# Performance work log

Hardware: AMD Instinct MI355X
Metric: run time of the kernel (lower is better)

Reference implementation:

```python
import jax, jax.numpy as jnp
import numpy as np
from jax import lax

IMG = 800.0      # image size (square)
STRIDE = 8       # FPN P3 stride
HF = 100; WF = 100; C = 256
A = 3            # anchors per location (aspect ratios 0.5,1,2)
PRE_NMS = 2000   # rpn_pre_nms_top_n_train
POST_NMS = 1000  # rpn_post_nms_top_n_test
NMS_TH = 0.7     # rpn_nms_thresh
POOL = 7; SR = 2 # ROIAlign output size / sampling ratio
NUM_CLASSES = 2
REP = 1024       # TwoMLPHead representation size
BBOX_CLAMP = float(np.log(1000.0 / 16.0))


def make_anchors():
    size = 64.0
    ratios = np.array([0.5, 1.0, 2.0])
    h = size * np.sqrt(ratios); w = size / np.sqrt(ratios)
    base = np.stack([-w / 2, -h / 2, w / 2, h / 2], 1)  # [A,4]
    sy = np.arange(HF) * STRIDE; sx = np.arange(WF) * STRIDE
    yy, xx = np.meshgrid(sy, sx, indexing='ij')
    shifts = np.stack([xx, yy, xx, yy], -1).reshape(-1, 1, 4)  # [H*W,1,4]
    return (shifts + base[None]).reshape(-1, 4).astype(np.float32)  # [H*W*A,4], (H,W,A) order


def conv2d(x, w, b, pad):
    y = lax.conv_general_dilated(x, w, (1, 1), pad, dimension_numbers=('NCHW', 'OIHW', 'NCHW'))
    return y + b[None, :, None, None]


def decode(deltas, anchors):
    wa = anchors[:, 2] - anchors[:, 0]; ha = anchors[:, 3] - anchors[:, 1]
    cxa = anchors[:, 0] + 0.5 * wa; cya = anchors[:, 1] + 0.5 * ha
    dw = jnp.minimum(deltas[:, 2], BBOX_CLAMP)
    dh = jnp.minimum(deltas[:, 3], BBOX_CLAMP)
    cx = deltas[:, 0] * wa + cxa; cy = deltas[:, 1] * ha + cya
    w = jnp.exp(dw) * wa; h = jnp.exp(dh) * ha
    return jnp.stack([cx - 0.5 * w, cy - 0.5 * h, cx + 0.5 * w, cy + 0.5 * h], 1)


def box_iou_one(box, boxes):
    lt = jnp.maximum(box[:2], boxes[:, :2]); rb = jnp.minimum(box[2:], boxes[:, 2:])
    wh = jnp.clip(rb - lt, 0.0)
    inter = wh[:, 0] * wh[:, 1]
    a1 = (box[2] - box[0]) * (box[3] - box[1])
    a2 = (boxes[:, 2] - boxes[:, 0]) * (boxes[:, 3] - boxes[:, 1])
    return inter / (a1 + a2 - inter + 1e-9)


def nms_fixed(boxes, scores, thresh, keep_n):
    order = jnp.argsort(-scores)
    b = boxes[order]; s = scores[order]
    n = b.shape[0]; ar = jnp.arange(n)
    def body(i, alive):
        sup = (box_iou_one(b[i], b) > thresh) & (ar > i) & alive[i]
        return alive & (~sup)
    alive = lax.fori_loop(0, n, body, jnp.ones((n,), bool))
    _, idx = lax.top_k(jnp.where(alive, s, -jnp.inf), keep_n)
    return b[idx]  # [keep_n,4]


def roi_align_one(feat, roi):
    # feat [C,Hf,Wf], roi [4] in image coords (x1,y1,x2,y2)
    Hf, Wf = feat.shape[1], feat.shape[2]
    x1, y1, x2, y2 = roi / STRIDE
    bw = (x2 - x1) / POOL; bh = (y2 - y1) / POOL
    k = (jnp.arange(POOL * SR) + 0.5) / SR  # [S]
    xs = jnp.clip(x1 + bw * k, 0.0, Wf - 1.0)
    ys = jnp.clip(y1 + bh * k, 0.0, Hf - 1.0)
    y0 = jnp.floor(ys); x0 = jnp.floor(xs)
    y0i = y0.astype(jnp.int32); x0i = x0.astype(jnp.int32)
    y1i = jnp.minimum(y0i + 1, Hf - 1); x1i = jnp.minimum(x0i + 1, Wf - 1)
    ly = ys - y0; lx = xs - x0; hy = 1.0 - ly; hx = 1.0 - lx
    v00 = feat[:, y0i[:, None], x0i[None, :]]
    v01 = feat[:, y0i[:, None], x1i[None, :]]
    v10 = feat[:, y1i[:, None], x0i[None, :]]
    v11 = feat[:, y1i[:, None], x1i[None, :]]
    out = ((hy[:, None] * hx[None, :]) * v00 + (hy[:, None] * lx[None, :]) * v01
           + (ly[:, None] * hx[None, :]) * v10 + (ly[:, None] * lx[None, :]) * v11)  # [C,S,S]
    return out.reshape(feat.shape[0], POOL, SR, POOL, SR).mean(axis=(2, 4))  # [C,7,7]


def _forward(features, rpn_conv_w, rpn_conv_b, rpn_cls_w, rpn_cls_b, rpn_bbox_w, rpn_bbox_b,
             fc1_w, fc1_b, fc2_w, fc2_b, cls_w, cls_b, reg_w, reg_b):
    B = features.shape[0]
    t = jax.nn.relu(conv2d(features, rpn_conv_w, rpn_conv_b, 'SAME'))
    obj = conv2d(t, rpn_cls_w, rpn_cls_b, 'VALID').transpose(0, 2, 3, 1).reshape(B, -1)  # (H,W,A)
    dl = (conv2d(t, rpn_bbox_w, rpn_bbox_b, 'VALID')
          .reshape(B, A, 4, HF, WF).transpose(0, 3, 4, 1, 2).reshape(B, -1, 4))
    anchors = jnp.asarray(make_anchors())

    def per_image(feat, o, d):
        s, idx = lax.top_k(o, PRE_NMS)
        boxes = jnp.clip(decode(d[idx], anchors[idx]), 0.0, IMG)
        rois = nms_fixed(boxes, s, NMS_TH, POST_NMS)
        return jax.vmap(lambda r: roi_align_one(feat, r))(rois)  # [K,C,7,7]

    pooled = jax.vmap(per_image)(features, obj, dl)  # [B,K,C,7,7]
    x = pooled.reshape(B, POST_NMS, -1)
    x = jax.nn.relu(x @ fc1_w + fc1_b)
    x = jax.nn.relu(x @ fc2_w + fc2_b)
    return jnp.concatenate([x @ cls_w + cls_b, x @ reg_w + reg_b], axis=-1)  # [B,K,10]


def setup_inputs() -> dict:
    key = jax.random.key(0)
    ks = jax.random.split(key, 8)
    def w(k, shape, s=0.01):
        return jax.random.normal(k, shape, jnp.float32) * s
    return {
        'features': jax.random.normal(ks[0], (2, C, HF, WF), jnp.float32),
        'rpn_conv_w': w(ks[1], (C, C, 3, 3)), 'rpn_conv_b': jnp.zeros((C,), jnp.float32),
        'rpn_cls_w': w(ks[2], (A, C, 1, 1)), 'rpn_cls_b': jnp.zeros((A,), jnp.float32),
        'rpn_bbox_w': w(ks[3], (4 * A, C, 1, 1)), 'rpn_bbox_b': jnp.zeros((4 * A,), jnp.float32),
        'fc1_w': w(ks[4], (C * POOL * POOL, REP)), 'fc1_b': jnp.zeros((REP,), jnp.float32),
        'fc2_w': w(ks[5], (REP, REP)), 'fc2_b': jnp.zeros((REP,), jnp.float32),
        'cls_w': w(ks[6], (REP, NUM_CLASSES)), 'cls_b': jnp.zeros((NUM_CLASSES,), jnp.float32),
        'reg_w': w(ks[7], (REP, 4 * NUM_CLASSES)), 'reg_b': jnp.zeros((4 * NUM_CLASSES,), jnp.float32),
    }


def reference(features, rpn_conv_w, rpn_conv_b, rpn_cls_w, rpn_cls_b, rpn_bbox_w, rpn_bbox_b,
              fc1_w, fc1_b, fc2_w, fc2_b, cls_w, cls_b, reg_w, reg_b):
    return _forward(features, rpn_conv_w, rpn_conv_b, rpn_cls_w, rpn_cls_b, rpn_bbox_w,
                    rpn_bbox_b, fc1_w, fc1_b, fc2_w, fc2_b, cls_w, cls_b, reg_w, reg_b)
```

## Files before the change

### kernel.cpp

```cpp
#include <hip/hip_runtime.h>
#include <hip/hip_bf16.h>
#include <math.h>

#define NPOS 10000
#define NANCH 30000
#define PRE 2000
#define POST 1000
#define RESQ 4096
#define CLAMPD 4.135166556742356
#define FPH 102
#define FPW 132

typedef __attribute__((ext_vector_type(8))) short bf16x8v;
typedef __attribute__((ext_vector_type(4))) float f32x4v;

__device__ __forceinline__ unsigned long long mapu64(double f) {
  unsigned long long b = (unsigned long long)__double_as_longlong(f);
  return (b & 0x8000000000000000ULL) ? ~b : (b | 0x8000000000000000ULL);
}
__device__ __forceinline__ unsigned mapu32(float f) {
  unsigned b = __float_as_uint(f);
  return (b & 0x80000000u) ? ~b : (b | 0x80000000u);
}

__device__ __forceinline__ void async_load16(const void* g, void* l) {
  __builtin_amdgcn_global_load_lds((const __attribute__((address_space(1))) void*)g,
                                   (__attribute__((address_space(3))) void*)l, 16, 0, 0);
}

__global__ void repack_w_k(const float* __restrict__ w, double* __restrict__ wT64r) {
  int tid = blockIdx.x * 256 + threadIdx.x;
  if (tid >= 589824) return;
  int co = tid / 2304;
  int rem = tid % 2304;
  int ci = rem / 9, tap = rem % 9;
  wT64r[((size_t)tap * 256 + ci) * 256 + co] = (double)w[tid];
}

__global__ void wbt_k(const float* __restrict__ w, __hip_bfloat16* __restrict__ wBt) {
  int i = blockIdx.x * 256 + threadIdx.x;
  if (i >= 589824) return;
  int tap = i >> 16;
  int co = (i >> 8) & 255;
  int ci = i & 255;
  wBt[i] = __float2bfloat16(w[(co * 256 + ci) * 9 + tap]);
}

__global__ void transpose_feat_k(const float* __restrict__ feat, float* __restrict__ featT) {
  __shared__ float tile[32][33];
  int b = blockIdx.z;
  int c0 = blockIdx.y * 32;
  int p0 = blockIdx.x * 32;
  int tx = threadIdx.x & 31, ty = threadIdx.x >> 5;
  for (int r = 0; r < 4; ++r) {
    int c = c0 + ty + r * 8, p = p0 + tx;
    tile[ty + r * 8][tx] = (p < NPOS) ? feat[((size_t)b * 256 + c) * NPOS + p] : 0.f;
  }
  __syncthreads();
  for (int r = 0; r < 4; ++r) {
    int p = p0 + ty + r * 8, c = c0 + tx;
    if (p < NPOS) featT[((size_t)b * NPOS + p) * 256 + c] = tile[tx][ty + r * 8];
  }
}

__global__ void fpad_zero_k(__hip_bfloat16* __restrict__ f) {
  size_t i = (size_t)blockIdx.x * 256 + threadIdx.x;
  uint4 z = {0, 0, 0, 0};
  ((uint4*)f)[i] = z;
}

__global__ void fpad_fill_k(const float* __restrict__ feat, __hip_bfloat16* __restrict__ fpadB) {
  __shared__ float tile[32][33];
  int b = blockIdx.z;
  int c0 = blockIdx.y * 32;
  int p0 = blockIdx.x * 32;
  int tx = threadIdx.x & 31, ty = threadIdx.x >> 5;
  for (int r = 0; r < 4; ++r) {
    int c = c0 + ty + r * 8, p = p0 + tx;
    tile[ty + r * 8][tx] = (p < NPOS) ? feat[((size_t)b * 256 + c) * NPOS + p] : 0.f;
  }
  __syncthreads();
  for (int r = 0; r < 4; ++r) {
    int p = p0 + ty + r * 8, c = c0 + tx;
    if (p < NPOS) {
      int y = p / 100, x = p % 100;
      fpadB[(((size_t)b * FPH + y + 1) * FPW + (x + 1)) * 256 + c] =
          __float2bfloat16(tile[tx][ty + r * 8]);
    }
  }
}

__global__ __launch_bounds__(256) void conv_mfma_k(const __hip_bfloat16* __restrict__ fpadB,
                                                   const __hip_bfloat16* __restrict__ wBt,
                                                   const float* __restrict__ bias,
                                                   float* __restrict__ t32) {
  __shared__ __hip_bfloat16 As[128 * 64];
  __shared__ __hip_bfloat16 Bs[128 * 64];
  const int t = threadIdx.x;
  const int wv = t >> 6;
  const int lane = t & 63;
  const int lr = lane & 15, lg = lane >> 4;
  const int wr = wv >> 1, wc = wv & 1;
  const int co0 = blockIdx.x * 128;
  const int mt = blockIdx.y;
  const int img = mt / 100;
  const int rem = mt % 100;
  const int y0 = (rem / 4) * 4, x0 = (rem % 4) * 32;

  f32x4v acc[4][4];
#pragma unroll
  for (int i = 0; i < 4; ++i)
#pragma unroll
    for (int j = 0; j < 4; ++j)
#pragma unroll
      for (int r = 0; r < 4; ++r) acc[i][j][r] = 0.f;

  int srow[4], sseg[4];
#pragma unroll
  for (int i = 0; i < 4; ++i) {
    int c = i * 256 + t;
    srow[i] = c >> 3;
    sseg[i] = (c & 7) ^ (srow[i] & 7);
  }
  int arow[4], brow[4], sk[2];
#pragma unroll
  for (int ms = 0; ms < 4; ++ms) arow[ms] = (wr * 64 + ms * 16 + lr) * 128;
#pragma unroll
  for (int ns = 0; ns < 4; ++ns) brow[ns] = (wc * 64 + ns * 16 + lr) * 128;
#pragma unroll
  for (int kk = 0; kk < 2; ++kk) sk[kk] = (((kk * 4 + lg) ^ (lr & 7)) * 16);

  for (int chunk = 0; chunk < 36; ++chunk) {
    int tap = chunk >> 2;
    int ci0 = (chunk & 3) * 64;
    int dy = tap / 3, dx = tap % 3;
    __syncthreads();
#pragma unroll
    for (int i = 0; i < 4; ++i) {
      int r = srow[i];
      int py = y0 + (r >> 5) + dy, px = x0 + (r & 31) + dx;
      const __hip_bfloat16* ga =
          fpadB + ((((size_t)img * FPH + py) * FPW + px) << 8) + ci0 + sseg[i] * 8;
      async_load16(ga, (char*)As + ((i * 256 + wv * 64) * 16));
    }
#pragma unroll
    for (int i = 0; i < 4; ++i) {
      int r = srow[i];
      const __hip_bfloat16* gb =
          wBt + ((size_t)(tap * 256 + co0 + r) << 8) + ci0 + sseg[i] * 8;
      async_load16(gb, (char*)Bs + ((i * 256 + wv * 64) * 16));
    }
    __syncthreads();

    bf16x8v af[2][4], bf[2][4];
#pragma unroll
    for (int kk = 0; kk < 2; ++kk) {
#pragma unroll
      for (int ms = 0; ms < 4; ++ms)
        af[kk][ms] = *(const bf16x8v*)((const char*)As + arow[ms] + sk[kk]);
#pragma unroll
      for (int ns = 0; ns < 4; ++ns)
        bf[kk][ns] = *(const bf16x8v*)((const char*)Bs + brow[ns] + sk[kk]);
    }
#pragma unroll
    for (int ms = 0; ms < 4; ++ms)
#pragma unroll
      for (int ns = 0; ns < 4; ++ns) {
        acc[ms][ns] = __builtin_amdgcn_mfma_f32_16x16x32_bf16(af[0][ms], bf[0][ns], acc[ms][ns], 0, 0, 0);
        acc[ms][ns] = __builtin_amdgcn_mfma_f32_16x16x32_bf16(af[1][ms], bf[1][ns], acc[ms][ns], 0, 0, 0);
      }
  }

#pragma unroll
  for (int ms = 0; ms < 4; ++ms) {
    int mbase = wr * 64 + ms * 16 + lg * 4;
#pragma unroll
    for (int ns = 0; ns < 4; ++ns) {
      int gn = co0 + wc * 64 + ns * 16 + lr;
      float bv = bias[gn];
#pragma unroll
      for (int r = 0; r < 4; ++r) {
        int m = mbase + r;
        int y = y0 + (m >> 5), x = x0 + (m & 31);
        if (x < 100)
          t32[((size_t)(img * NPOS + y * 100 + x)) * 256 + gn] = fmaxf(acc[ms][ns][r] + bv, 0.f);
      }
    }
  }
}

__global__ void rpn_obj_k(const float* __restrict__ t32, const float* __restrict__ wcls,
                          const float* __restrict__ bcls, float* __restrict__ obj) {
  __shared__ float wl[3][256];
  int tid = threadIdx.x;
  for (int i = tid; i < 768; i += 256) wl[i / 256][i % 256] = wcls[i];
  __syncthreads();
  int gp = blockIdx.x * 256 + tid;
  if (gp >= 2 * NPOS) return;
  const float* tr = t32 + (size_t)gp * 256;
  float a0 = 0.f, a1 = 0.f, a2 = 0.f;
  for (int c = 0; c < 256; c += 4) {
    float4 v = *(const float4*)&tr[c];
    a0 += v.x * wl[0][c] + v.y * wl[0][c + 1] + v.z * wl[0][c + 2] + v.w * wl[0][c + 3];
    a1 += v.x * wl[1][c] + v.y * wl[1][c + 1] + v.z * wl[1][c + 2] + v.w * wl[1][c + 3];
    a2 += v.x * wl[2][c] + v.y * wl[2][c + 1] + v.z * wl[2][c + 2] + v.w * wl[2][c + 3];
  }
  int b = gp / NPOS, lp = gp % NPOS;
  obj[(size_t)b * NANCH + lp * 3 + 0] = a0 + bcls[0];
  obj[(size_t)b * NANCH + lp * 3 + 1] = a1 + bcls[1];
  obj[(size_t)b * NANCH + lp * 3 + 2] = a2 + bcls[2];
}

__global__ __launch_bounds__(1024) void select_k(const float* __restrict__ obj,
                                                 unsigned* __restrict__ cand,
                                                 int* __restrict__ poslist,
                                                 int* __restrict__ counts, float delta) {
  int b = blockIdx.x;
  __shared__ unsigned hist[16][256];
  __shared__ unsigned posbm[320];
  __shared__ unsigned sh_prefix, sh_rem;
  __shared__ int sh_ac, sh_pc;
  int tid = threadIdx.x;
  int wid = tid >> 6;
  const float* ob = obj + (size_t)b * NANCH;

  if (tid == 0) { sh_prefix = 0; sh_rem = PRE; sh_ac = 0; sh_pc = 0; }
  for (int i = tid; i < 320; i += 1024) posbm[i] = 0;
  for (int shift = 24; shift >= 0; shift -= 8) {
    for (int i = tid; i < 16 * 256; i += 1024) ((unsigned*)hist)[i] = 0;
    __syncthreads();
    unsigned pref = sh_prefix;
    unsigned himask = (shift == 24) ? 0u : (0xFFFFFFFFu << (shift + 8));
    for (int i = tid; i < NANCH; i += 1024) {
      unsigned u = mapu32(ob[i]);
      if ((u & himask) == pref) atomicAdd(&hist[wid][(u >> shift) & 255], 1u);
    }
    __syncthreads();
    if (tid < 256) {
      unsigned s = hist[0][tid];
      for (int w = 1; w < 16; ++w) s += hist[w][tid];
      hist[0][tid] = s;
    }
    __syncthreads();
    if (tid == 0) {
      unsigned rem = sh_rem, pfx = sh_prefix;
      for (int bb = 255; bb >= 0; --bb) {
        unsigned c = hist[0][bb];
        if (rem > c) rem -= c;
        else { pfx |= ((unsigned)bb) << shift; break; }
      }
      sh_prefix = pfx; sh_rem = rem;
    }
    __syncthreads();
  }
  unsigned T = sh_prefix;
  float Tval = __uint_as_float((T & 0x80000000u) ? (T & 0x7FFFFFFFu) : ~T);
  float thr = Tval - delta;
  for (int i = tid; i < NANCH; i += 1024) {
    if (ob[i] >= thr) {
      int p = atomicAdd(&sh_ac, 1);
      if (p < RESQ) cand[(size_t)b * RESQ + p] = (unsigned)i;
      int pos = i / 3;
      atomicOr(&posbm[pos >> 5], 1u << (pos & 31));
    }
  }
  __syncthreads();
  for (int w = tid; w < 313; w += 1024) {
    unsigned word = posbm[w];
    while (word) {
      int bit = __builtin_ctz(word);
      word &= word - 1;
      int q = atomicAdd(&sh_pc, 1);
      if (q < RESQ) poslist[(size_t)b * RESQ + q] = w * 32 + bit;
    }
  }
  __syncthreads();
  if (tid == 0) {
    counts[b * 2 + 0] = min(sh_ac, RESQ);
    counts[b * 2 + 1] = min(sh_pc, RESQ);
  }
}

__global__ __launch_bounds__(256) void rescore_t3_k(const float* __restrict__ featT,
                                                    const double* __restrict__ wT64r,
                                                    const int* __restrict__ poslist,
                                                    const int* __restrict__ counts,
                                                    double* __restrict__ t64p) {
  int z = blockIdx.z;
  int b = z / 3, tg = z % 3;
  int cnt = counts[b * 2 + 1];
  int mbase = blockIdx.y * 64;
  if (mbase >= cnt) return;
  int co0 = blockIdx.x * 64;
  __shared__ double As[32][66];
  __shared__ double Bs[32][66];
  __shared__ int sgy[64], sgx[64];
  int tid = threadIdx.x;
  int tx = tid & 15;
  int ty = tid >> 4;
  if (tid < 64) {
    int q = mbase + tid;
    int pos = poslist[(size_t)b * RESQ + (q < cnt ? q : (cnt - 1))];
    sgy[tid] = pos / 100;
    sgx[tid] = pos % 100;
  }
  __syncthreads();
  const float* fb = featT + (size_t)b * NPOS * 256;

  double acc[4][4] = {};
  int ar = tid >> 2, aq = tid & 3;
  int bk = tid >> 3, bq = tid & 7;

  for (int tt = 0; tt < 3; ++tt) {
    int tap = tg * 3 + tt;
    int dy = tap / 3 - 1, dx = tap % 3 - 1;
    for (int cc = 0; cc < 8; ++cc) {
      int ci0 = cc * 32;
      __syncthreads();
      {
        int gy = sgy[ar] + dy, gx = sgx[ar] + dx;
        float4 v0 = {0.f, 0.f, 0.f, 0.f}, v1 = {0.f, 0.f, 0.f, 0.f};
        if (gy >= 0 && gy < 100 && gx >= 0 && gx < 100) {
          const float* fp = &fb[(size_t)(gy * 100 + gx) * 256 + ci0 + aq * 8];
          v0 = *(const float4*)fp;
          v1 = *(const float4*)(fp + 4);
        }
        As[aq * 8 + 0][ar] = (double)v0.x;
        As[aq * 8 + 1][ar] = (double)v0.y;
        As[aq * 8 + 2][ar] = (double)v0.z;
        As[aq * 8 + 3][ar] = (double)v0.w;
        As[aq * 8 + 4][ar] = (double)v1.x;
        As[aq * 8 + 5][ar] = (double)v1.y;
        As[aq * 8 + 6][ar] = (double)v1.z;
        As[aq * 8 + 7][ar] = (double)v1.w;
      }
      {
        const double* gw = wT64r + ((size_t)(tap * 256 + ci0 + bk)) * 256 + co0 + bq * 8;
#pragma unroll
        for (int i = 0; i < 4; ++i)
          *(double2*)&Bs[bk][bq * 8 + i * 2] = *(const double2*)(gw + i * 2);
      }
      __syncthreads();
#pragma unroll
      for (int kk = 0; kk < 32; ++kk) {
        double2 a01 = *(const double2*)&As[kk][ty * 4];
        double2 a23 = *(const double2*)&As[kk][ty * 4 + 2];
        double b0 = Bs[kk][tx];
        double b1 = Bs[kk][tx + 16];
        double b2 = Bs[kk][tx + 32];
        double b3 = Bs[kk][tx + 48];
        acc[0][0] += a01.x * b0; acc[0][1] += a01.x * b1;
        acc[0][2] += a01.x * b2; acc[0][3] += a01.x * b3;
        acc[1][0] += a01.y * b0; acc[1][1] += a01.y * b1;
        acc[1][2] += a01.y * b2; acc[1][3] += a01.y * b3;
        acc[2][0] += a23.x * b0; acc[2][1] += a23.x * b1;
        acc[2][2] += a23.x * b2; acc[2][3] += a23.x * b3;
        acc[3][0] += a23.y * b0; acc[3][1] += a23.y * b1;
        acc[3][2] += a23.y * b2; acc[3][3] += a23.y * b3;
      }
    }
  }
#pragma unroll
  for (int p = 0; p < 4; ++p) {
    int gp = mbase + ty * 4 + p;
    if (gp >= cnt) continue;
    double* outp = t64p + (((size_t)tg * 2 + b) * RESQ + gp) * 256 + co0;
#pragma unroll
    for (int j = 0; j < 4; ++j) outp[tx + 16 * j] = acc[p][j];
  }
}

__global__ __launch_bounds__(256) void rescore_heads_k(const double* __restrict__ t64p,
                                                       const float* __restrict__ bias,
                                                       const int* __restrict__ poslist,
                                                       const int* __restrict__ counts,
                                                       const float* __restrict__ wcls,
                                                       const float* __restrict__ bcls,
                                                       const float* __restrict__ wbbox,
                                                       const float* __restrict__ bbbox,
                                                       double* __restrict__ obj64,
                                                       double* __restrict__ deltas64) {
  int b = blockIdx.y;
  int cnt = counts[b * 2 + 1];
  int base = blockIdx.x * 16;
  if (base >= cnt) return;
  int tid = threadIdx.x;
  if (tid >= 240) return;
  int pp = tid / 15, j = tid % 15;
  int gp = base + pp;
  if (gp >= cnt) return;
  int pos = poslist[(size_t)b * RESQ + gp];
  const double* p0 = t64p + (((size_t)0 * 2 + b) * RESQ + gp) * 256;
  const double* p1 = t64p + (((size_t)1 * 2 + b) * RESQ + gp) * 256;
  const double* p2 = t64p + (((size_t)2 * 2 + b) * RESQ + gp) * 256;
  const float* wr = (j < 3) ? (wcls + j * 256) : (wbbox + (j - 3) * 256);
  double acc = 0.0;
  for (int c = 0; c < 256; ++c) {
    double tv = fmax(p0[c] + p1[c] + p2[c] + (double)bias[c], 0.0);
    acc += tv * (double)wr[c];
  }
  if (j < 3) {
    obj64[(size_t)b * NANCH + pos * 3 + j] = acc + (double)bcls[j];
  } else {
    int jj = j - 3;
    int a = jj >> 2, kk = jj & 3;
    deltas64[((size_t)b * NANCH + pos * 3 + a) * 4 + kk] = acc + (double)bbbox[jj];
  }
}

__global__ __launch_bounds__(1024) void topk_decode_k(const unsigned* __restrict__ cand,
                                                      const int* __restrict__ counts,
                                                      const double* __restrict__ obj64,
                                                      const double* __restrict__ deltas64,
                                                      double* __restrict__ boxesd,
                                                      float* __restrict__ boxesf) {
  int b = blockIdx.x;
  __shared__ unsigned long long selk[RESQ];
  __shared__ unsigned seli[RESQ];
  int tid = threadIdx.x;
  int acnt = counts[b * 2 + 0];
  for (int s = tid; s < RESQ; s += 1024) {
    if (s < acnt) {
      unsigned idx = cand[(size_t)b * RESQ + s];
      selk[s] = mapu64(obj64[(size_t)b * NANCH + idx]);
      seli[s] = idx;
    } else {
      selk[s] = 0ULL;
      seli[s] = 0xFFFFFFFFu;
    }
  }
  __syncthreads();
  for (unsigned k = 2; k <= RESQ; k <<= 1) {
    for (unsigned j = k >> 1; j > 0; j >>= 1) {
      for (int i = tid; i < RESQ; i += 1024) {
        int l = i ^ (int)j;
        if (l > i) {
          unsigned long long ka = selk[i], kb = selk[l];
          unsigned ia = seli[i], ib = seli[l];
          bool before_lb = (kb > ka) || (kb == ka && ib < ia);
          bool asc = ((i & (int)k) == 0);
          if (asc == before_lb) {
            selk[i] = kb; selk[l] = ka;
            seli[i] = ib; seli[l] = ia;
          }
        }
      }
      __syncthreads();
    }
  }
  const double ratios[3] = {0.5, 1.0, 2.0};
  for (int p = tid; p < PRE; p += 1024) {
    unsigned idx = seli[p];
    int a = (int)(idx % 3u);
    int pos = (int)(idx / 3u);
    int ypix = pos / 100, xpix = pos % 100;
    double sx = (double)(xpix * 8), sy = (double)(ypix * 8);
    double sq = sqrt(ratios[a]);
    double w2 = (64.0 / sq) * 0.5;
    double h2 = (64.0 * sq) * 0.5;
    float x1a = (float)(sx - w2), y1a = (float)(sy - h2);
    float x2a = (float)(sx + w2), y2a = (float)(sy + h2);
    double wa = (double)x2a - (double)x1a;
    double ha = (double)y2a - (double)y1a;
    double cxa = (double)x1a + 0.5 * wa, cya = (double)y1a + 0.5 * ha;
    const double* dd = deltas64 + ((size_t)b * NANCH + idx) * 4;
    double dx = dd[0], dy = dd[1];
    double dw = fmin(dd[2], CLAMPD), dh = fmin(dd[3], CLAMPD);
    double cx = dx * wa + cxa, cy = dy * ha + cya;
    double w = exp(dw) * wa, h = exp(dh) * ha;
    double bx1 = fmin(fmax(cx - 0.5 * w, 0.0), 800.0);
    double by1 = fmin(fmax(cy - 0.5 * h, 0.0), 800.0);
    double bx2 = fmin(fmax(cx + 0.5 * w, 0.0), 800.0);
    double by2 = fmin(fmax(cy + 0.5 * h, 0.0), 800.0);
    double* bo = boxesd + ((size_t)b * PRE + p) * 4;
    bo[0] = bx1; bo[1] = by1; bo[2] = bx2; bo[3] = by2;
    float* bf = boxesf + ((size_t)b * PRE + p) * 4;
    bf[0] = (float)bx1; bf[1] = (float)by1; bf[2] = (float)bx2; bf[3] = (float)by2;
  }
}

__global__ void supmat_k(const double* __restrict__ boxes, unsigned* __restrict__ sup) {
  int b = blockIdx.y;
  int gt = blockIdx.x * 256 + threadIdx.x;
  int i = gt >> 6, w = gt & 63;
  if (i >= PRE) return;
  const double* bb = boxes + (size_t)b * PRE * 4;
  double x1 = bb[i * 4 + 0], y1 = bb[i * 4 + 1], x2 = bb[i * 4 + 2], y2 = bb[i * 4 + 3];
  double a1 = (x2 - x1) * (y2 - y1);
  unsigned m = 0;
  int j0 = w * 32;
  for (int jj = 0; jj < 32; ++jj) {
    int j = j0 + jj;
    if (j >= PRE) break;
    if (j > i) {
      double u1 = bb[j * 4 + 0], v1 = bb[j * 4 + 1], u2 = bb[j * 4 + 2], v2 = bb[j * 4 + 3];
      double ltx = fmax(x1, u1), lty = fmax(y1, v1);
      double rbx = fmin(x2, u2), rby = fmin(y2, v2);
      double ww = fmax(rbx - ltx, 0.0), hh = fmax(rby - lty, 0.0);
      double inter = ww * hh;
      double a2 = (u2 - u1) * (v2 - v1);
      double iou = inter / (a1 + a2 - inter + 1e-9);
      if (iou > 0.7) m |= 1u << jj;
    }
  }
  sup[((size_t)b * 2048 + i) * 64 + w] = m;
}

__global__ void nms_emit_k(const unsigned* __restrict__ sup, const float* __restrict__ boxes,
                           float* __restrict__ rois) {
  int b = blockIdx.x;
  int tid = threadIdx.x;
  __shared__ unsigned buf[2][4096];
  __shared__ unsigned aw_s[64];
  __shared__ unsigned pre[64];
  __shared__ unsigned sh_m;
  const unsigned* sb = sup + (size_t)b * 2048 * 64;

  for (int i = tid; i < 4096; i += 256) buf[0][i] = sb[i];
  __syncthreads();

  unsigned aw = 0;
  if (tid < 64) aw = (tid < 62) ? 0xFFFFFFFFu : (tid == 62 ? 0xFFFFu : 0u);

  for (int c = 0; c < 32; ++c) {
    if (tid >= 64 && c + 1 < 32) {
      for (int i = tid - 64; i < 4096; i += 192) buf[(c + 1) & 1][i] = sb[(size_t)(c + 1) * 4096 + i];
    }
    if (tid < 64) {
      const unsigned* B = buf[c & 1];
      unsigned rlo = B[tid * 64 + 2 * c];
      unsigned rhi = B[tid * 64 + 2 * c + 1];
      unsigned clo = __shfl(aw, 2 * c);
      unsigned chi = __shfl(aw, 2 * c + 1);
      unsigned long long cm = (unsigned long long)clo | ((unsigned long long)chi << 32);
      unsigned long long m = cm;
      while (m) {
        int ii = __builtin_ctzll(m);
        unsigned long long kd = (unsigned long long)__shfl(rlo, ii) |
                                ((unsigned long long)__shfl(rhi, ii) << 32);
        cm &= ~kd;
        m = cm & ~((2ULL << ii) - 1ULL);
      }
      unsigned kill = 0;
      unsigned long long m2 = cm;
      while (m2) {
        int i0 = __builtin_ctzll(m2); m2 &= m2 - 1;
        int i1 = -1, i2 = -1, i3 = -1;
        if (m2) { i1 = __builtin_ctzll(m2); m2 &= m2 - 1; }
        if (m2) { i2 = __builtin_ctzll(m2); m2 &= m2 - 1; }
        if (m2) { i3 = __builtin_ctzll(m2); m2 &= m2 - 1; }
        unsigned k0 = B[i0 * 64 + tid];
        unsigned k1 = (i1 >= 0) ? B[i1 * 64 + tid] : 0u;
        unsigned k2 = (i2 >= 0) ? B[i2 * 64 + tid] : 0u;
        unsigned k3 = (i3 >= 0) ? B[i3 * 64 + tid] : 0u;
        kill |= (k0 | k1) | (k2 | k3);
      }
      aw &= ~kill;
    }
    __syncthreads();
  }
  if (tid < 64) aw_s[tid] = aw;
  __syncthreads();
  if (tid == 0) {
    unsigned m = 0;
    for (int w = 0; w < 64; ++w) { pre[w] = m; m += __popc(aw_s[w]); }
    sh_m = m;
  }
  __syncthreads();
  unsigned m = sh_m;
  for (int i = tid; i < PRE; i += 256) {
    int w = i >> 5;
    unsigned word = aw_s[w];
    unsigned lower = word & ((1u << (i & 31)) - 1u);
    unsigned rank = pre[w] + __popc(lower);
    bool al = (word >> (i & 31)) & 1u;
    unsigned dst;
    if (al) {
      if (rank >= POST) continue;
      dst = rank;
    } else {
      unsigned dpos = m + ((unsigned)i - rank);
      if (dpos >= POST) continue;
      dst = dpos;
    }
    const float4 v = *(const float4*)(boxes + ((size_t)b * PRE + i) * 4);
    *(float4*)(rois + ((size_t)b * POST + dst) * 4) = v;
  }
}

__global__ void roi_align_k(const float* __restrict__ featT, const float* __restrict__ rois,
                            __hip_bfloat16* __restrict__ pooled) {
  __shared__ float slx[14], sly[14];
  __shared__ int sx0[14], sx1[14], sy0[14], sy1[14];
  int tid = threadIdx.x;
  int gro = blockIdx.x;
  int b = gro / POST;
  const float* r = rois + (size_t)gro * 4;
  if (tid < 14) {
    float x1 = r[0] * 0.125f, x2 = r[2] * 0.125f;
    float bw = (x2 - x1) / 7.0f;
    float k = ((float)tid + 0.5f) / 2.0f;
    float xs = fminf(fmaxf(x1 + bw * k, 0.f), 99.f);
    float x0f = floorf(xs);
    int x0i = (int)x0f;
    sx0[tid] = x0i; sx1[tid] = min(x0i + 1, 99); slx[tid] = xs - x0f;
  } else if (tid < 28) {
    int s = tid - 14;
    float y1 = r[1] * 0.125f, y2 = r[3] * 0.125f;
    float bh = (y2 - y1) / 7.0f;
    float k = ((float)s + 0.5f) / 2.0f;
    float ys = fminf(fmaxf(y1 + bh * k, 0.f), 99.f);
    float y0f = floorf(ys);
    int y0i = (int)y0f;
    sy0[s] = y0i; sy1[s] = min(y0i + 1, 99); sly[s] = ys - y0f;
  }
  __syncthreads();
  int c = tid;
  const float* fb = featT + (size_t)b * NPOS * 256 + c;
  __hip_bfloat16* outp = pooled + (size_t)gro * 12544 + (size_t)c * 49;
  for (int ph = 0; ph < 7; ++ph) {
    for (int pw = 0; pw < 7; ++pw) {
      float acc = 0.f;
#pragma unroll
      for (int sy = 0; sy < 2; ++sy) {
        int yi = ph * 2 + sy;
        int y0 = sy0[yi], y1 = sy1[yi];
        float ly = sly[yi], hy = 1.f - ly;
#pragma unroll
        for (int sx = 0; sx < 2; ++sx) {
          int xi = pw * 2 + sx;
          int x0 = sx0[xi], x1 = sx1[xi];
          float lx = slx[xi], hx = 1.f - lx;
          float v00 = fb[(size_t)(y0 * 100 + x0) * 256];
          float v01 = fb[(size_t)(y0 * 100 + x1) * 256];
          float v10 = fb[(size_t)(y1 * 100 + x0) * 256];
          float v11 = fb[(size_t)(y1 * 100 + x1) * 256];
          acc += hy * hx * v00 + hy * lx * v01 + ly * hx * v10 + ly * lx * v11;
        }
      }
      outp[ph * 7 + pw] = __float2bfloat16(acc * 0.25f);
    }
  }
}

__global__ void wt_bf16_k(const float* __restrict__ w, __hip_bfloat16* __restrict__ wt,
                          int K, int N) {
  __shared__ float tile[32][33];
  int k0 = blockIdx.x * 32, n0 = blockIdx.y * 32;
  int tx = threadIdx.x & 31, ty = threadIdx.x >> 5;
  for (int r = 0; r < 4; ++r)
    tile[ty + r * 8][tx] = w[(size_t)(k0 + ty + r * 8) * N + n0 + tx];
  __syncthreads();
  for (int r = 0; r < 4; ++r)
    wt[(size_t)(n0 + ty + r * 8) * K + k0 + tx] = __float2bfloat16(tile[tx][ty + r * 8]);
}

__global__ __launch_bounds__(256) void gemm_bf16_k(const __hip_bfloat16* __restrict__ A,
                                                   const __hip_bfloat16* __restrict__ Bt,
                                                   const float* __restrict__ bias,
                                                   __hip_bfloat16* __restrict__ C,
                                                   int N, int K, int relu) {
  __shared__ __hip_bfloat16 As[128 * 64];
  __shared__ __hip_bfloat16 Bs[128 * 64];
  const int t = threadIdx.x;
  const int w = t >> 6;
  const int lane = t & 63;
  const int lr = lane & 15, lg = lane >> 4;
  const int wr = w >> 1, wc = w & 1;
  const int m0 = blockIdx.y * 128, n0 = blockIdx.x * 128;

  f32x4v acc[4][4];
#pragma unroll
  for (int i = 0; i < 4; ++i)
#pragma unroll
    for (int j = 0; j < 4; ++j)
#pragma unroll
      for (int r = 0; r < 4; ++r) acc[i][j][r] = 0.f;

  int srow[4], soff[4];
#pragma unroll
  for (int i = 0; i < 4; ++i) {
    int c = i * 256 + t;
    int row = c >> 3, ccd = c & 7;
    srow[i] = row;
    soff[i] = (ccd ^ (row & 7)) * 8;
  }
  int arow[4], brow[4], sk[2];
#pragma unroll
  for (int ms = 0; ms < 4; ++ms) arow[ms] = (wr * 64 + ms * 16 + lr) * 128;
#pragma unroll
  for (int ns = 0; ns < 4; ++ns) brow[ns] = (wc * 64 + ns * 16 + lr) * 128;
#pragma unroll
  for (int kk = 0; kk < 2; ++kk) sk[kk] = (((kk * 4 + lg) ^ (lr & 7)) * 16);

  for (int k0 = 0; k0 < K; k0 += 64) {
    __syncthreads();
#pragma unroll
    for (int i = 0; i < 4; ++i) {
      const __hip_bfloat16* ga = A + (size_t)(m0 + srow[i]) * K + k0 + soff[i];
      async_load16(ga, (char*)As + ((i * 256 + w * 64) * 16));
    }
#pragma unroll
    for (int i = 0; i < 4; ++i) {
      const __hip_bfloat16* gb = Bt + (size_t)(n0 + srow[i]) * K + k0 + soff[i];
      async_load16(gb, (char*)Bs + ((i * 256 + w * 64) * 16));
    }
    __syncthreads();

    bf16x8v af[2][4], bf[2][4];
#pragma unroll
    for (int kk = 0; kk < 2; ++kk) {
#pragma unroll
      for (int ms = 0; ms < 4; ++ms)
        af[kk][ms] = *(const bf16x8v*)((const char*)As + arow[ms] + sk[kk]);
#pragma unroll
      for (int ns = 0; ns < 4; ++ns)
        bf[kk][ns] = *(const bf16x8v*)((const char*)Bs + brow[ns] + sk[kk]);
    }
#pragma unroll
    for (int ms = 0; ms < 4; ++ms)
#pragma unroll
      for (int ns = 0; ns < 4; ++ns) {
        acc[ms][ns] = __builtin_amdgcn_mfma_f32_16x16x32_bf16(af[0][ms], bf[0][ns], acc[ms][ns], 0, 0, 0);
        acc[ms][ns] = __builtin_amdgcn_mfma_f32_16x16x32_bf16(af[1][ms], bf[1][ns], acc[ms][ns], 0, 0, 0);
      }
  }

#pragma unroll
  for (int ms = 0; ms < 4; ++ms) {
    int gm = m0 + wr * 64 + ms * 16 + lg * 4;
#pragma unroll
    for (int ns = 0; ns < 4; ++ns) {
      int gn = n0 + wc * 64 + ns * 16 + lr;
      float bv = bias[gn];
#pragma unroll
      for (int r = 0; r < 4; ++r) {
        float v = acc[ms][ns][r] + bv;
        if (relu) v = fmaxf(v, 0.f);
        C[(size_t)(gm + r) * N + gn] = __float2bfloat16(v);
      }
    }
  }
}

#define FC1K 12544
#define FC1KS 2
#define FC1KSEG (FC1K / FC1KS)
__global__ __launch_bounds__(256) void gemm_part_k(const __hip_bfloat16* __restrict__ A,
                                                   const __hip_bfloat16* __restrict__ Bt,
                                                   float* __restrict__ part) {
  __shared__ __hip_bfloat16 As[128 * 64];
  __shared__ __hip_bfloat16 Bs[64 * 64];
  const int t = threadIdx.x;
  const int w = t >> 6;
  const int lane = t & 63;
  const int lr = lane & 15, lg = lane >> 4;
  const int wr = w >> 1, wc = w & 1;
  const int m0 = blockIdx.y * 128, n0 = blockIdx.x * 64;
  const int ks = blockIdx.z;
  const int kbase = ks * FC1KSEG;

  f32x4v acc[4][2];
#pragma unroll
  for (int i = 0; i < 4; ++i)
#pragma unroll
    for (int j = 0; j < 2; ++j)
#pragma unroll
      for (int r = 0; r < 4; ++r) acc[i][j][r] = 0.f;

  int srow[4], soff[4];
#pragma unroll
  for (int i = 0; i < 4; ++i) {
    int c = i * 256 + t;
    int row = c >> 3, ccd = c & 7;
    srow[i] = row;
    soff[i] = (ccd ^ (row & 7)) * 8;
  }
  int arow[4], brow[2], sk[2];
#pragma unroll
  for (int ms = 0; ms < 4; ++ms) arow[ms] = (wr * 64 + ms * 16 + lr) * 128;
#pragma unroll
  for (int ns = 0; ns < 2; ++ns) brow[ns] = (wc * 32 + ns * 16 + lr) * 128;
#pragma unroll
  for (int kk = 0; kk < 2; ++kk) sk[kk] = (((kk * 4 + lg) ^ (lr & 7)) * 16);

  for (int k0 = 0; k0 < FC1KSEG; k0 += 64) {
    __syncthreads();
#pragma unroll
    for (int i = 0; i < 4; ++i) {
      const __hip_bfloat16* ga = A + (size_t)(m0 + srow[i]) * FC1K + kbase + k0 + soff[i];
      async_load16(ga, (char*)As + ((i * 256 + w * 64) * 16));
    }
#pragma unroll
    for (int i = 0; i < 2; ++i) {
      const __hip_bfloat16* gb = Bt + (size_t)(n0 + srow[i]) * FC1K + kbase + k0 + soff[i];
      async_load16(gb, (char*)Bs + ((i * 256 + w * 64) * 16));
    }
    __syncthreads();

    bf16x8v af[2][4], bf[2][2];
#pragma unroll
    for (int kk = 0; kk < 2; ++kk) {
#pragma unroll
      for (int ms = 0; ms < 4; ++ms)
        af[kk][ms] = *(const bf16x8v*)((const char*)As + arow[ms] + sk[kk]);
#pragma unroll
      for (int ns = 0; ns < 2; ++ns)
        bf[kk][ns] = *(const bf16x8v*)((const char*)Bs + brow[ns] + sk[kk]);
    }
#pragma unroll
    for (int ms = 0; ms < 4; ++ms)
#pragma unroll
      for (int ns = 0; ns < 2; ++ns) {
        acc[ms][ns] = __builtin_amdgcn_mfma_f32_16x16x32_bf16(af[0][ms], bf[0][ns], acc[ms][ns], 0, 0, 0);
        acc[ms][ns] = __builtin_amdgcn_mfma_f32_16x16x32_bf16(af[1][ms], bf[1][ns], acc[ms][ns], 0, 0, 0);
      }
  }

  float* pb = part + (size_t)ks * 2048 * 1024;
#pragma unroll
  for (int ms = 0; ms < 4; ++ms) {
    int gm = m0 + wr * 64 + ms * 16 + lg * 4;
#pragma unroll
    for (int ns = 0; ns < 2; ++ns) {
      int gn = n0 + wc * 32 + ns * 16 + lr;
#pragma unroll
      for (int r = 0; r < 4; ++r)
        pb[(size_t)(gm + r) * 1024 + gn] = acc[ms][ns][r];
    }
  }
}

__global__ void reduce_bias_relu_k(const float* __restrict__ part, const float* __restrict__ bias,
                                   __hip_bfloat16* __restrict__ x1) {
  int i4 = blockIdx.x * 256 + threadIdx.x;
  if (i4 >= 524288) return;
  const float4 a = ((const float4*)part)[i4];
  const float4 b = ((const float4*)part)[524288 + i4];
  const float4 bv = ((const float4*)bias)[i4 & 255];
  float v0 = fmaxf(a.x + b.x + bv.x, 0.f);
  float v1 = fmaxf(a.y + b.y + bv.y, 0.f);
  float v2 = fmaxf(a.z + b.z + bv.z, 0.f);
  float v3 = fmaxf(a.w + b.w + bv.w, 0.f);
  __hip_bfloat16* o = x1 + (size_t)i4 * 4;
  o[0] = __float2bfloat16(v0);
  o[1] = __float2bfloat16(v1);
  o[2] = __float2bfloat16(v2);
  o[3] = __float2bfloat16(v3);
}

__global__ void final_heads_k(const __hip_bfloat16* __restrict__ x2,
                              const float* __restrict__ cls_w, const float* __restrict__ cls_b,
                              const float* __restrict__ reg_w, const float* __restrict__ reg_b,
                              float* __restrict__ out) {
  __shared__ float wl[1024][10];
  int tid = threadIdx.x;
  for (int i = tid; i < 1024 * 10; i += 256) {
    int k = i / 10, n = i % 10;
    wl[k][n] = (n < 2) ? cls_w[k * 2 + n] : reg_w[k * 8 + (n - 2)];
  }
  __syncthreads();
  int gt = blockIdx.x * 256 + tid;
  if (gt >= 2 * POST * 10) return;
  int mg = gt / 10, n = gt % 10;
  const __hip_bfloat16* xr = x2 + (size_t)mg * 1024;
  float acc = 0.f;
  for (int k = 0; k < 1024; ++k) acc += __bfloat162float(xr[k]) * wl[k][n];
  acc += (n < 2) ? cls_b[n] : reg_b[n - 2];
  out[(size_t)mg * 10 + n] = acc;
}

extern "C" void kernel_launch(void* const* d_in, const int* in_sizes, int n_in,
                              void* d_out, int out_size, void* d_ws, size_t ws_size,
                              hipStream_t stream) {
  const float* features   = (const float*)d_in[0];
  const float* rpn_conv_w = (const float*)d_in[1];
  const float* rpn_conv_b = (const float*)d_in[2];
  const float* rpn_cls_w  = (const float*)d_in[3];
  const float* rpn_cls_b  = (const float*)d_in[4];
  const float* rpn_bbox_w = (const float*)d_in[5];
  const float* rpn_bbox_b = (const float*)d_in[6];
  const float* fc1_w = (const float*)d_in[7];
  const float* fc1_b = (const float*)d_in[8];
  const float* fc2_w = (const float*)d_in[9];
  const float* fc2_b = (const float*)d_in[10];
  const float* cls_w = (const float*)d_in[11];
  const float* cls_b = (const float*)d_in[12];
  const float* reg_w = (const float*)d_in[13];
  const float* reg_b = (const float*)d_in[14];
  float* out = (float*)d_out;

  char* ws = (char*)d_ws;
  size_t off = 0;
  auto alloc = [&](size_t bytes) -> void* {
    off = (off + 255) & ~(size_t)255;
    void* p = ws + off;
    off += bytes;
    return p;
  };
  float* featT = (float*)alloc((size_t)2 * NPOS * 256 * 4);
  float* rois  = (float*)alloc((size_t)2 * POST * 4 * 4);
  __hip_bfloat16* w1t = (__hip_bfloat16*)alloc((size_t)1024 * 12544 * 2);
  __hip_bfloat16* w2t = (__hip_bfloat16*)alloc((size_t)1024 * 1024 * 2);
  __hip_bfloat16* x1  = (__hip_bfloat16*)alloc((size_t)2048 * 1024 * 2);
  __hip_bfloat16* x2  = (__hip_bfloat16*)alloc((size_t)2048 * 1024 * 2);
  off = (off + 255) & ~(size_t)255;
  size_t region = off;
  double*   wT64r    = (double*)alloc((size_t)589824 * 8);
  __hip_bfloat16* fpadB = (__hip_bfloat16*)alloc((size_t)2 * FPH * FPW * 256 * 2);
  __hip_bfloat16* wBt   = (__hip_bfloat16*)alloc((size_t)589824 * 2);
  off = (off + 255) & ~(size_t)255;
  size_t uni = off;
  float*  t32  = (float*)(ws + uni);
  float*  objf = (float*)(ws + uni + (((size_t)2 * NPOS * 256 * 4 + 255) & ~(size_t)255));
  double* t64p = (double*)(ws + uni);
  size_t uni_sz = (size_t)3 * 2 * RESQ * 256 * 8;
  off = uni + uni_sz;
  double*   obj64    = (double*)alloc((size_t)2 * NANCH * 8);
  double*   deltas64 = (double*)alloc((size_t)2 * NANCH * 4 * 8);
  double*   boxesd   = (double*)alloc((size_t)2 * PRE * 4 * 8);
  float*    boxesf   = (float*)alloc((size_t)2 * PRE * 4 * 4);
  unsigned* sup      = (unsigned*)alloc((size_t)2 * 2048 * 64 * 4);
  unsigned* cand     = (unsigned*)alloc((size_t)2 * RESQ * 4);
  int*      poslist  = (int*)alloc((size_t)2 * RESQ * 4);
  int*      counts   = (int*)alloc(64);
  __hip_bfloat16* pooled = (__hip_bfloat16*)(ws + region);
  size_t pooled_sz = (size_t)2048 * 12544 * 2;
  float* fc1part = (float*)(ws + region + ((pooled_sz + 255) & ~(size_t)255));
  size_t part_end = region + ((pooled_sz + 255) & ~(size_t)255) + (size_t)FC1KS * 2048 * 1024 * 4;
  if (off < part_end) off = part_end;
  (void)ws_size; (void)in_sizes; (void)n_in; (void)out_size;

  repack_w_k<<<2304, 256, 0, stream>>>(rpn_conv_w, wT64r);
  wbt_k<<<2304, 256, 0, stream>>>(rpn_conv_w, wBt);
  transpose_feat_k<<<dim3(313, 8, 2), 256, 0, stream>>>(features, featT);
  fpad_zero_k<<<3366, 256, 0, stream>>>(fpadB);
  fpad_fill_k<<<dim3(313, 8, 2), 256, 0, stream>>>(features, fpadB);
  conv_mfma_k<<<dim3(2, 200), 256, 0, stream>>>(fpadB, wBt, rpn_conv_b, t32);
  rpn_obj_k<<<79, 256, 0, stream>>>(t32, rpn_cls_w, rpn_cls_b, objf);
  select_k<<<2, 1024, 0, stream>>>(objf, cand, poslist, counts, 8e-3f);
  rescore_t3_k<<<dim3(4, RESQ / 64, 6), 256, 0, stream>>>(featT, wT64r, poslist, counts, t64p);
  rescore_heads_k<<<dim3(RESQ / 16, 2), 256, 0, stream>>>(t64p, rpn_conv_b, poslist, counts,
                                                          rpn_cls_w, rpn_cls_b, rpn_bbox_w,
                                                          rpn_bbox_b, obj64, deltas64);
  topk_decode_k<<<2, 1024, 0, stream>>>(cand, counts, obj64, deltas64, boxesd, boxesf);
  supmat_k<<<dim3(512, 2), 256, 0, stream>>>(boxesd, sup);
  nms_emit_k<<<2, 256, 0, stream>>>(sup, boxesf, rois);
  wt_bf16_k<<<dim3(392, 32), 256, 0, stream>>>(fc1_w, w1t, 12544, 1024);
  wt_bf16_k<<<dim3(32, 32), 256, 0, stream>>>(fc2_w, w2t, 1024, 1024);
  roi_align_k<<<2 * POST, 256, 0, stream>>>(featT, rois, pooled);
  gemm_part_k<<<dim3(16, 16, FC1KS), 256, 0, stream>>>(pooled, w1t, fc1part);
  reduce_bias_relu_k<<<2048, 256, 0, stream>>>(fc1part, fc1_b, x1);
  gemm_bf16_k<<<dim3(8, 16), 256, 0, stream>>>(x1, w2t, fc2_b, x2, 1024, 1024, 1);
  final_heads_k<<<79, 256, 0, stream>>>(x2, cls_w, cls_b, reg_w, reg_b, out);
}
```

Baseline: 1.033 ms.

## Split NMS kill-mask accumulation across all four wavefronts in nms_emit_k

The per-chunk kill-mask OR over surviving rows is now spread round-robin over all four wavefronts, with the partial masks reduced through shared memory. Previously a single wavefront did this while the other three only prefetched. The shuffles are also replaced by readlane/readfirstlane scalar reads. This shortens the serial per-chunk critical path but adds two extra block barriers per chunk, and prefetching now overlaps only the in-chunk resolve step.

```diff
diff --git a/kernel.cpp b/kernel.cpp
--- a/kernel.cpp
+++ b/kernel.cpp
@@ -510,57 +510,59 @@
                            float* __restrict__ rois) {
   int b = blockIdx.x;
   int tid = threadIdx.x;
+  int wv = tid >> 6, lane = tid & 63;
   __shared__ unsigned buf[2][4096];
+  __shared__ unsigned kill_s[4][64];
   __shared__ unsigned aw_s[64];
+  __shared__ unsigned sh_cm0, sh_cm1;
   __shared__ unsigned pre[64];
   __shared__ unsigned sh_m;
   const unsigned* sb = sup + (size_t)b * 2048 * 64;
 
   for (int i = tid; i < 4096; i += 256) buf[0][i] = sb[i];
-  __syncthreads();
-
-  unsigned aw = 0;
-  if (tid < 64) aw = (tid < 62) ? 0xFFFFFFFFu : (tid == 62 ? 0xFFFFu : 0u);
+  if (tid < 64) aw_s[tid] = (tid < 62) ? 0xFFFFFFFFu : (tid == 62 ? 0xFFFFu : 0u);
+  __syncthreads();
 
   for (int c = 0; c < 32; ++c) {
-    if (tid >= 64 && c + 1 < 32) {
-      for (int i = tid - 64; i < 4096; i += 192) buf[(c + 1) & 1][i] = sb[(size_t)(c + 1) * 4096 + i];
-    }
-    if (tid < 64) {
-      const unsigned* B = buf[c & 1];
-      unsigned rlo = B[tid * 64 + 2 * c];
-      unsigned rhi = B[tid * 64 + 2 * c + 1];
-      unsigned clo = __shfl(aw, 2 * c);
-      unsigned chi = __shfl(aw, 2 * c + 1);
+    const unsigned* B = buf[c & 1];
+    if (wv == 0) {
+      unsigned rlo = B[lane * 64 + 2 * c];
+      unsigned rhi = B[lane * 64 + 2 * c + 1];
+      unsigned clo = __builtin_amdgcn_readfirstlane(aw_s[2 * c]);
+      unsigned chi = __builtin_amdgcn_readfirstlane(aw_s[2 * c + 1]);
       unsigned long long cm = (unsigned long long)clo | ((unsigned long long)chi << 32);
       unsigned long long m = cm;
       while (m) {
         int ii = __builtin_ctzll(m);
-        unsigned long long kd = (unsigned long long)__shfl(rlo, ii) |
-                                ((unsigned long long)__shfl(rhi, ii) << 32);
+        unsigned klo = (unsigned)__builtin_amdgcn_readlane((int)rlo, ii);
+        unsigned khi = (unsigned)__builtin_amdgcn_readlane((int)rhi, ii);
+        unsigned long long kd = (unsigned long long)klo | ((unsigned long long)khi << 32);
         cm &= ~kd;
         m = cm & ~((2ULL << ii) - 1ULL);
       }
-      unsigned kill = 0;
+      if (lane == 0) { sh_cm0 = (unsigned)cm; sh_cm1 = (unsigned)(cm >> 32); }
+    } else if (c + 1 < 32) {
+      for (int i = tid - 64; i < 4096; i += 192) buf[(c + 1) & 1][i] = sb[(size_t)(c + 1) * 4096 + i];
+    }
+    __syncthreads();
+    {
+      unsigned long long cm = (unsigned long long)sh_cm0 | ((unsigned long long)sh_cm1 << 32);
+      unsigned k = 0;
       unsigned long long m2 = cm;
+      int cnt = 0;
       while (m2) {
-        int i0 = __builtin_ctzll(m2); m2 &= m2 - 1;
-        int i1 = -1, i2 = -1, i3 = -1;
-        if (m2) { i1 = __builtin_ctzll(m2); m2 &= m2 - 1; }
-        if (m2) { i2 = __builtin_ctzll(m2); m2 &= m2 - 1; }
-        if (m2) { i3 = __builtin_ctzll(m2); m2 &= m2 - 1; }
-        unsigned k0 = B[i0 * 64 + tid];
-        unsigned k1 = (i1 >= 0) ? B[i1 * 64 + tid] : 0u;
-        unsigned k2 = (i2 >= 0) ? B[i2 * 64 + tid] : 0u;
-        unsigned k3 = (i3 >= 0) ? B[i3 * 64 + tid] : 0u;
-        kill |= (k0 | k1) | (k2 | k3);
-      }
-      aw &= ~kill;
-    }
-    __syncthreads();
-  }
-  if (tid < 64) aw_s[tid] = aw;
-  __syncthreads();
+        int ii = __builtin_ctzll(m2);
+        m2 &= m2 - 1;
+        if ((cnt & 3) == wv) k |= B[ii * 64 + lane];
+        ++cnt;
+      }
+      kill_s[wv][lane] = k;
+    }
+    __syncthreads();
+    if (tid < 64)
+      aw_s[tid] &= ~(kill_s[0][tid] | kill_s[1][tid] | kill_s[2][tid] | kill_s[3][tid]);
+    __syncthreads();
+  }
   if (tid == 0) {
     unsigned m = 0;
     for (int w = 0; w < 64; ++w) { pre[w] = m; m += __popc(aw_s[w]); }
```

After: 974.0 us. 1.06x faster.
